# Optimization experiments

Hardware: AMD Instinct MI355X
Metric: run time of the kernel (lower is better)

The kernel has to match this reference:

```python
import jax, jax.numpy as jnp
import numpy as np

HIDDEN = 1024
HEADS = 16
HEAD_DIM = HIDDEN // HEADS
ROPE_BASE = 10000.0


def rope_cos_sin(seq_len, head_dim, dtype=jnp.float32):
    inv_freq = 1.0 / (ROPE_BASE ** (jnp.arange(0, head_dim, 2, dtype=jnp.float32) / head_dim))
    t = jnp.arange(seq_len, dtype=jnp.float32)
    freqs = jnp.einsum('i,j->ij', t, inv_freq)          # [L, head_dim/2]
    emb = jnp.concatenate([freqs, freqs], axis=-1)       # [L, head_dim]
    return emb.astype(dtype), jnp.cos(emb).astype(dtype), jnp.sin(emb).astype(dtype)


def rotate_half(x):
    half = x.shape[-1] // 2
    return jnp.concatenate([-x[..., half:], x[..., :half]], axis=-1)


def setup_inputs() -> dict:
    key = jax.random.key(0)
    kx, kq, kk, kv, ko = jax.random.split(key, 5)
    B, L = 4, 2048
    scale = 1.0 / np.sqrt(HIDDEN)
    x = jax.random.normal(kx, (B, L, HIDDEN), dtype=jnp.float32)
    Wq = jax.random.normal(kq, (HIDDEN, HIDDEN), dtype=jnp.float32) * scale
    Wk = jax.random.normal(kk, (HIDDEN, HIDDEN), dtype=jnp.float32) * scale
    Wv = jax.random.normal(kv, (HIDDEN, HIDDEN), dtype=jnp.float32) * scale
    Wo = jax.random.normal(ko, (HIDDEN, HIDDEN), dtype=jnp.float32) * scale
    return {"x": x, "Wq": Wq, "Wk": Wk, "Wv": Wv, "Wo": Wo}


def reference(x, Wq, Wk, Wv, Wo):
    B, L, D = x.shape
    H, Hd = HEADS, HEAD_DIM
    # projections (nn.Linear: y = x @ W.T; weights here stored already as [out,in])
    q = (x @ Wq.T).reshape(B, L, H, Hd).transpose(0, 2, 1, 3)  # [B,H,L,Hd]
    k = (x @ Wk.T).reshape(B, L, H, Hd).transpose(0, 2, 1, 3)
    v = (x @ Wv.T).reshape(B, L, H, Hd).transpose(0, 2, 1, 3)
    _, cos, sin = rope_cos_sin(L, Hd, x.dtype)                  # [L, Hd]
    cos = cos[None, None, :, :]
    sin = sin[None, None, :, :]
    q = q * cos + rotate_half(q) * sin
    k = k * cos + rotate_half(k) * sin
    scores = jnp.einsum('bhqd,bhkd->bhqk', q, k) / np.sqrt(Hd)  # [B,H,L,L]
    attn = jax.nn.softmax(scores, axis=-1)
    out = jnp.einsum('bhqk,bhkd->bhqd', attn, v)                # [B,H,L,Hd]
    out = out.transpose(0, 2, 1, 3).reshape(B, L, D)
    return out @ Wo.T
```

## Files before the change

### kernel.cpp

```cpp
#include <hip/hip_runtime.h>
#include <math.h>

#define BB 4
#define LL 2048
#define DD 1024
#define HH 16
#define HD 64
#define BL (BB*LL)

typedef __attribute__((ext_vector_type(8))) short bf16x8;
typedef __attribute__((ext_vector_type(4))) short bf16x4;
typedef __attribute__((ext_vector_type(4))) float f32x4;

__device__ inline short f2bf(float f) {
    union { float f; unsigned u; } v; v.f = f;
    unsigned r = v.u + 0x7fffu + ((v.u >> 16) & 1u);
    return (short)(r >> 16);
}

__device__ inline unsigned pk_bf16(float a, float b) {
    union { float f; unsigned u; } x, y; x.f = a; y.f = b;
#if __has_builtin(__builtin_amdgcn_perm)
    return __builtin_amdgcn_perm(y.u, x.u, 0x07060302u);
#else
    return (x.u >> 16) | (y.u & 0xffff0000u);
#endif
}

__device__ inline float exp2x(float x) {
#if __has_builtin(__builtin_amdgcn_exp2f)
    return __builtin_amdgcn_exp2f(x);
#else
    return exp2f(x);
#endif
}

__device__ inline void gload_lds16(const void* g, void* l) {
    __builtin_amdgcn_global_load_lds(
        (const __attribute__((address_space(1))) unsigned int*)g,
        (__attribute__((address_space(3))) unsigned int*)l, 16, 0, 0);
}

#define NB_CASTX ((BL*DD)/2048)
#define NB_CASTW (4*((DD*DD)/2048))
#define NB_ROPE  256

__global__ __launch_bounds__(256) void prep_kernel(
    const float* __restrict__ x,
    const float* __restrict__ w0, const float* __restrict__ w1,
    const float* __restrict__ w2, const float* __restrict__ w3,
    short* __restrict__ xb, short* __restrict__ wout,
    float2* __restrict__ tab)
{
    const int bid = blockIdx.x;
    if (bid < NB_CASTX) {
        int i = (bid * 256 + threadIdx.x) * 8;
        float4 a = *(const float4*)(x + i);
        float4 b = *(const float4*)(x + i + 4);
        bf16x8 o;
        o[0]=f2bf(a.x); o[1]=f2bf(a.y); o[2]=f2bf(a.z); o[3]=f2bf(a.w);
        o[4]=f2bf(b.x); o[5]=f2bf(b.y); o[6]=f2bf(b.z); o[7]=f2bf(b.w);
        *(bf16x8*)(xb + i) = o;
    } else if (bid < NB_CASTX + NB_CASTW) {
        const int nw_blocks = (DD*DD) / 2048;
        int b2  = bid - NB_CASTX;
        int sel = b2 / nw_blocks;
        int blk = b2 % nw_blocks;
        const float* in = (sel == 0) ? w0 : (sel == 1) ? w1 : (sel == 2) ? w2 : w3;
        int i = (blk * 256 + threadIdx.x) * 8;
        float4 a = *(const float4*)(in + i);
        float4 b = *(const float4*)(in + i + 4);
        bf16x8 o;
        o[0]=f2bf(a.x); o[1]=f2bf(a.y); o[2]=f2bf(a.z); o[3]=f2bf(a.w);
        o[4]=f2bf(b.x); o[5]=f2bf(b.y); o[6]=f2bf(b.z); o[7]=f2bf(b.w);
        *(bf16x8*)(wout + (size_t)sel * DD * DD + i) = o;
    } else {
        int idx = (bid - NB_CASTX - NB_CASTW) * 256 + threadIdx.x;
        int lq = idx >> 5, f = idx & 31;
        float inv = __expf((float)f * (-9.210340371976184f / 32.0f));
        float s, c;
        sincosf((float)lq * inv, &s, &c);
        tab[idx] = make_float2(c, s);
    }
}

__device__ inline void gemm_bt_128(const short* __restrict__ A,
                                   const short* __restrict__ B,
                                   short* Ash, short* Bsh,
                                   int i0, int n0, f32x4 (&acc)[4][4])
{
    const int t  = threadIdx.x;
    const int w  = t >> 6;
    const int l  = t & 63;
    const int g  = (t >> 4) & 3;
    const int ln = t & 15;
    const int rh = (w >> 1) * 64;
    const int ch = (w & 1) * 64;
    const int srow = w * 8 + (l >> 3);
    const int skol = ((l & 7) ^ (l >> 3)) * 8;
    const int rsw  = 8 * (ln & 7);

    for (int k0 = 0; k0 < DD; k0 += 64) {
        __syncthreads();
        const short* ga = A + (size_t)(i0 + srow) * DD + k0 + skol;
        const short* gb = B + (size_t)(n0 + srow) * DD + k0 + skol;
        short* la = Ash + w * 512;
        short* lb = Bsh + w * 512;
        #pragma unroll
        for (int j = 0; j < 4; ++j) {
            gload_lds16(ga + j * 32 * DD, la + j * 2048);
            gload_lds16(gb + j * 32 * DD, lb + j * 2048);
        }
        __syncthreads();

        #pragma unroll
        for (int kk = 0; kk < 2; ++kk) {
            bf16x8 af[4], bfr[4];
            #pragma unroll
            for (int mi = 0; mi < 4; ++mi)
                af[mi] = *(const bf16x8*)(Ash + (rh + mi*16 + ln)*64 + ((kk*32 + 8*g) ^ rsw));
            #pragma unroll
            for (int nj = 0; nj < 4; ++nj)
                bfr[nj] = *(const bf16x8*)(Bsh + (ch + nj*16 + ln)*64 + ((kk*32 + 8*g) ^ rsw));
            #pragma unroll
            for (int mi = 0; mi < 4; ++mi)
                #pragma unroll
                for (int nj = 0; nj < 4; ++nj)
                    acc[mi][nj] = __builtin_amdgcn_mfma_f32_16x16x32_bf16(
                        af[mi], bfr[nj], acc[mi][nj], 0, 0, 0);
        }
    }
}

__global__ __launch_bounds__(256, 4) void qkv_mfma_kernel(
    const short* __restrict__ xb, const short* __restrict__ Wqb,
    const short* __restrict__ Wkb, const short* __restrict__ Wvb,
    const float2* __restrict__ rope_tab,
    short* __restrict__ Qo, short* __restrict__ Ko, short* __restrict__ Vo)
{
    __shared__ short Ash[128*64];
    __shared__ short Bsh[128*64];

    const int gid = blockIdx.x;
    const int r8  = gid & 7;
    const int u   = gid >> 3;
    const int i_idx = r8 * 8 + (u & 7);
    const int nz  = u >> 3;
    const int n_idx = nz & 7;
    const int z   = nz >> 3;

    const short* Wm = (z == 0) ? Wqb : ((z == 1) ? Wkb : Wvb);
    const int i0 = i_idx * 128;
    const int n0 = n_idx * 128;

    f32x4 acc[4][4];
    #pragma unroll
    for (int mi = 0; mi < 4; ++mi)
        #pragma unroll
        for (int nj = 0; nj < 4; ++nj) acc[mi][nj] = (f32x4){0.f,0.f,0.f,0.f};

    gemm_bt_128(xb, Wm, Ash, Bsh, i0, n0, acc);

    const int t  = threadIdx.x;
    const int w  = t >> 6;
    const int g  = (t >> 4) & 3;
    const int ln = t & 15;
    const int rh = (w >> 1) * 64;

    if (z == 2) {
        short* buf = Ash;
        const int b = i0 >> 11, l0 = i0 & (LL - 1);
        const int d = t >> 2;
        const int c = t & 3;
        const int dk = d & 7;
        #pragma unroll
        for (int hp = 0; hp < 2; ++hp) {
            __syncthreads();
            if ((w & 1) == hp) {
                #pragma unroll
                for (int nj = 0; nj < 4; ++nj)
                    #pragma unroll
                    for (int mi = 0; mi < 4; ++mi)
                        #pragma unroll
                        for (int r = 0; r < 4; ++r)
                            buf[(nj*16 + ln)*136 + rh + mi*16 + 4*g + r]
                                = f2bf(acc[mi][nj][r]);
            }
            __syncthreads();
            short* dst = Vo + ((size_t)((b*HH + n_idx*2 + hp)*HD + d)) * LL + l0;
            #pragma unroll
            for (int j = 0; j < 4; ++j) {
                const short* src = buf + d*136 + c*8 + j*32;
                bf16x4 lo = *(const bf16x4*)(src);
                bf16x4 hi = *(const bf16x4*)(src + 4);
                const int tb = (j >> 1) * 64;
                const int hb = j & 1;
                const int aa = c >> 1;
                const int g0 = (c & 1) * 2;
                const int gi1 = 2*g0 + hb;
                *(bf16x4*)(dst + tb + ((gi1     ^ dk) << 3) + aa*4) = lo;
                *(bf16x4*)(dst + tb + (((gi1+2) ^ dk) << 3) + aa*4) = hi;
            }
        }
    } else {
        const int h = n_idx * 2 + (w & 1);
        short* Om = (z == 0) ? Qo : Ko;
        const float sc = (z == 0) ? 0.180336880111112f : 1.0f;
        const int gi0 = ln >> 3;
        const int wi  = ln & 7;
        #pragma unroll
        for (int mi = 0; mi < 4; ++mi)
            #pragma unroll
            for (int r = 0; r < 4; ++r) {
                int i = i0 + rh + mi*16 + 4*g + r;
                int b = i >> 11, lq = i & (LL - 1);
                float2 cs0 = rope_tab[lq*32 + ln];
                float2 cs1 = rope_tab[lq*32 + ln + 16];
                float r0 = (acc[mi][0][r]*cs0.x - acc[mi][2][r]*cs0.y) * sc;
                float r2 = (acc[mi][2][r]*cs0.x + acc[mi][0][r]*cs0.y) * sc;
                float r1 = (acc[mi][1][r]*cs1.x - acc[mi][3][r]*cs1.y) * sc;
                float r3 = (acc[mi][3][r]*cs1.x + acc[mi][1][r]*cs1.y) * sc;
                size_t base = ((size_t)(b*HH + h) * LL + lq) * HD;
                int xk = (z == 0) ? 0 : ((4*g + r) & 7);
                Om[base + (((gi0    ) ^ xk) << 3) + wi] = f2bf(r0);
                Om[base + (((gi0 + 2) ^ xk) << 3) + wi] = f2bf(r1);
                Om[base + (((gi0 + 4) ^ xk) << 3) + wi] = f2bf(r2);
                Om[base + (((gi0 + 6) ^ xk) << 3) + wi] = f2bf(r3);
            }
    }
}

__global__ __launch_bounds__(256) void attn_kernel(
    const short* __restrict__ Q, const short* __restrict__ K,
    const short* __restrict__ VT, short* __restrict__ AO)
{
    __shared__ short Ksh[64*64];
    __shared__ short VTs[64*64];

    const int t  = threadIdx.x;
    const int w  = t >> 6;
    const int l  = t & 63;
    const int g  = l >> 4;
    const int ln = l & 15;

    const int bh = blockIdx.x;
    const int q0 = blockIdx.y * 128;
    const short* Qb  = Q  + ((size_t)bh * LL + q0 + w*32) * HD;
    const short* Kb  = K  + (size_t)bh * LL * HD;
    const short* VTb = VT + (size_t)bh * HD * LL;

    bf16x8 qb[2][2];
    #pragma unroll
    for (int qi = 0; qi < 2; ++qi) {
        qb[qi][0] = *(const bf16x8*)(Qb + (size_t)(qi*16 + ln)*HD + 8*g);
        qb[qi][1] = *(const bf16x8*)(Qb + (size_t)(qi*16 + ln)*HD + 32 + 8*g);
    }

    const bf16x8 ONES = { (short)0x3F80, (short)0x3F80, (short)0x3F80, (short)0x3F80,
                          (short)0x3F80, (short)0x3F80, (short)0x3F80, (short)0x3F80 };

    f32x4 O[2][4];
    #pragma unroll
    for (int qi = 0; qi < 2; ++qi)
        #pragma unroll
        for (int db = 0; db < 4; ++db) O[qi][db] = (f32x4){0.f,0.f,0.f,0.f};
    f32x4 lsum[2];
    lsum[0] = (f32x4){0.f,0.f,0.f,0.f};
    lsum[1] = (f32x4){0.f,0.f,0.f,0.f};

    const int srow = l >> 3;
    const int scol = (l & 7) * 8;
    short* kdst = Ksh + w*1024;
    short* vdst = VTs + w*1024;
    const int lx = ln & 7;

    for (int kt = 0; kt < LL; kt += 64) {
        __syncthreads();
        const short* gk = Kb  + (size_t)(kt + w*16 + srow)*HD + scol;
        const short* gv = VTb + (size_t)(w*16 + srow)*LL + kt + scol;
        gload_lds16(gk,        kdst);
        gload_lds16(gk + 8*HD, kdst + 512);
        gload_lds16(gv,        vdst);
        gload_lds16(gv + 8*LL, vdst + 512);
        __syncthreads();

        unsigned pf[2][4][2];
        #pragma unroll
        for (int kb = 0; kb < 4; ++kb) {
            bf16x8 ka0 = *(const bf16x8*)(Ksh + (kb*16 + ln)*64 + ((g       ^ lx) << 3));
            bf16x8 ka1 = *(const bf16x8*)(Ksh + (kb*16 + ln)*64 + (((g + 4) ^ lx) << 3));
            #pragma unroll
            for (int qi = 0; qi < 2; ++qi) {
                f32x4 S = (f32x4){0.f,0.f,0.f,0.f};
                S = __builtin_amdgcn_mfma_f32_16x16x32_bf16(ka0, qb[qi][0], S, 0, 0, 0);
                S = __builtin_amdgcn_mfma_f32_16x16x32_bf16(ka1, qb[qi][1], S, 0, 0, 0);
                float p0 = exp2x(S[0]), p1 = exp2x(S[1]);
                float p2 = exp2x(S[2]), p3 = exp2x(S[3]);
                pf[qi][kb][0] = pk_bf16(p0, p1);
                pf[qi][kb][1] = pk_bf16(p2, p3);
            }
        }

        bf16x8 pa[2][2];
        #pragma unroll
        for (int qi = 0; qi < 2; ++qi)
            #pragma unroll
            for (int hb = 0; hb < 2; ++hb) {
                union { unsigned u[4]; bf16x8 v; } a;
                a.u[0] = pf[qi][2*hb][0];   a.u[1] = pf[qi][2*hb][1];
                a.u[2] = pf[qi][2*hb+1][0]; a.u[3] = pf[qi][2*hb+1][1];
                pa[qi][hb] = a.v;
            }

        #pragma unroll
        for (int hb = 0; hb < 2; ++hb) {
            lsum[0] = __builtin_amdgcn_mfma_f32_16x16x32_bf16(pa[0][hb], ONES, lsum[0], 0, 0, 0);
            lsum[1] = __builtin_amdgcn_mfma_f32_16x16x32_bf16(pa[1][hb], ONES, lsum[1], 0, 0, 0);
        }

        #pragma unroll
        for (int hb = 0; hb < 2; ++hb) {
            #pragma unroll
            for (int db = 0; db < 4; ++db) {
                bf16x8 vf = *(const bf16x8*)(VTs + (db*16 + ln)*64 + (((2*g + hb) ^ lx) << 3));
                O[0][db] = __builtin_amdgcn_mfma_f32_16x16x32_bf16(pa[0][hb], vf, O[0][db], 0, 0, 0);
                O[1][db] = __builtin_amdgcn_mfma_f32_16x16x32_bf16(pa[1][hb], vf, O[1][db], 0, 0, 0);
            }
        }
    }

    const int b = bh >> 4, h = bh & 15;
    #pragma unroll
    for (int qi = 0; qi < 2; ++qi) {
        #pragma unroll
        for (int r = 0; r < 4; ++r) {
            float inv = 1.0f / lsum[qi][r];
            int q = q0 + w*32 + qi*16 + 4*g + r;
            size_t base = ((size_t)(b*LL + q)) * DD + h*HD;
            #pragma unroll
            for (int db = 0; db < 4; ++db)
                AO[base + db*16 + ln] = f2bf(O[qi][db][r] * inv);
        }
    }
}

__global__ __launch_bounds__(256, 4) void oproj_mfma_kernel(
    const short* __restrict__ A, const short* __restrict__ Wob,
    float* __restrict__ out)
{
    __shared__ short Ash[128*64];
    __shared__ short Bsh[128*64];

    const int gid = blockIdx.x;
    const int r8  = gid & 7;
    const int u   = gid >> 3;
    const int i_idx = r8 * 8 + (u & 7);
    const int n_idx = u >> 3;
    const int i0 = i_idx * 128;
    const int n0 = n_idx * 128;

    f32x4 acc[4][4];
    #pragma unroll
    for (int mi = 0; mi < 4; ++mi)
        #pragma unroll
        for (int nj = 0; nj < 4; ++nj) acc[mi][nj] = (f32x4){0.f,0.f,0.f,0.f};

    gemm_bt_128(A, Wob, Ash, Bsh, i0, n0, acc);

    const int t  = threadIdx.x;
    const int w  = t >> 6;
    const int g  = (t >> 4) & 3;
    const int ln = t & 15;
    const int rh = (w >> 1) * 64;
    const int ch = (w & 1) * 64;

    #pragma unroll
    for (int mi = 0; mi < 4; ++mi)
        #pragma unroll
        for (int r = 0; r < 4; ++r) {
            size_t base = (size_t)(i0 + rh + mi*16 + 4*g + r) * DD + n0 + ch;
            #pragma unroll
            for (int nj = 0; nj < 4; ++nj)
                out[base + nj*16 + ln] = acc[mi][nj][r];
        }
}

extern "C" void kernel_launch(void* const* d_in, const int* in_sizes, int n_in,
                              void* d_out, int out_size, void* d_ws, size_t ws_size,
                              hipStream_t stream) {
    const float* x  = (const float*)d_in[0];
    const float* Wq = (const float*)d_in[1];
    const float* Wk = (const float*)d_in[2];
    const float* Wv = (const float*)d_in[3];
    const float* Wo = (const float*)d_in[4];
    float* out = (float*)d_out;

    const size_t n_x = (size_t)BL * DD;
    const size_t n_w = (size_t)DD * DD;
    short* xb  = (short*)d_ws;
    short* Wqb = xb  + n_x;
    short* Wkb = Wqb + n_w;
    short* Wvb = Wkb + n_w;
    short* Wob = Wvb + n_w;
    short* Q   = Wob + n_w;
    short* K   = Q   + n_x;
    short* VTg = K   + n_x;
    short* AOb = VTg + n_x;
    float2* tab = (float2*)(AOb + n_x);

    prep_kernel<<<NB_CASTX + NB_CASTW + NB_ROPE, 256, 0, stream>>>(
        x, Wq, Wk, Wv, Wo, xb, Wqb, tab);

    qkv_mfma_kernel<<<1536, 256, 0, stream>>>(xb, Wqb, Wkb, Wvb, tab, Q, K, VTg);

    dim3 g2(BB*HH, LL/128);
    attn_kernel<<<g2, 256, 0, stream>>>(Q, K, VTg, AOb);

    oproj_mfma_kernel<<<512, 256, 0, stream>>>(AOb, Wob, out);
}
```

Measured before the change: 251.9 us.

## Double-buffer GEMM K-loop in LDS with 32-wide stages to overlap loads

Reworks the shared bf16 GEMM main loop used by the QKV and output projections. It now keeps two 32-column K stages in LDS and issues the global-to-LDS loads for the next stage before computing on the current one, so load latency overlaps with MFMA work. LDS use stays the same because the two 128x64 tiles become four 128x32 tiles. The XOR swizzle is dropped in favour of a plain 32-short row stride, which may add LDS bank conflicts on the fragment reads. The number of barriers per 64-wide K step stays at two, but each barrier now covers half the work.

```diff
diff --git a/kernel.cpp b/kernel.cpp
--- a/kernel.cpp
+++ b/kernel.cpp
@@ -84,9 +84,40 @@
     }
 }
 
+__device__ inline void stage32(const short* __restrict__ A,
+                               const short* __restrict__ B,
+                               short* la, short* lb,
+                               int i0, int n0, int k0, int srow, int scol)
+{
+    const short* ga = A + (size_t)(i0 + srow) * DD + k0 + scol;
+    const short* gb = B + (size_t)(n0 + srow) * DD + k0 + scol;
+    gload_lds16(ga,           la);
+    gload_lds16(ga + 16 * DD, la + 512);
+    gload_lds16(gb,           lb);
+    gload_lds16(gb + 16 * DD, lb + 512);
+}
+
+__device__ inline void comp32(const short* Ab, const short* Bb,
+                              int rh, int ch, int g, int ln, f32x4 (&acc)[4][4])
+{
+    bf16x8 af[4], bfr[4];
+    #pragma unroll
+    for (int mi = 0; mi < 4; ++mi)
+        af[mi] = *(const bf16x8*)(Ab + (rh + mi*16 + ln)*32 + 8*g);
+    #pragma unroll
+    for (int nj = 0; nj < 4; ++nj)
+        bfr[nj] = *(const bf16x8*)(Bb + (ch + nj*16 + ln)*32 + 8*g);
+    #pragma unroll
+    for (int mi = 0; mi < 4; ++mi)
+        #pragma unroll
+        for (int nj = 0; nj < 4; ++nj)
+            acc[mi][nj] = __builtin_amdgcn_mfma_f32_16x16x32_bf16(
+                af[mi], bfr[nj], acc[mi][nj], 0, 0, 0);
+}
+
 __device__ inline void gemm_bt_128(const short* __restrict__ A,
                                    const short* __restrict__ B,
-                                   short* Ash, short* Bsh,
+                                   short* S,
                                    int i0, int n0, f32x4 (&acc)[4][4])
 {
     const int t  = threadIdx.x;
@@ -96,39 +127,23 @@
     const int ln = t & 15;
     const int rh = (w >> 1) * 64;
     const int ch = (w & 1) * 64;
-    const int srow = w * 8 + (l >> 3);
-    const int skol = ((l & 7) ^ (l >> 3)) * 8;
-    const int rsw  = 8 * (ln & 7);
-
+    const int srow = w * 32 + (l >> 2);
+    const int scol = (l & 3) * 8;
+
+    short* A0 = S;           short* A1 = S + 4096;
+    short* B0 = S + 8192;    short* B1 = S + 12288;
+    short* la0 = A0 + w*1024; short* la1 = A1 + w*1024;
+    short* lb0 = B0 + w*1024; short* lb1 = B1 + w*1024;
+
+    stage32(A, B, la0, lb0, i0, n0, 0, srow, scol);
     for (int k0 = 0; k0 < DD; k0 += 64) {
         __syncthreads();
-        const short* ga = A + (size_t)(i0 + srow) * DD + k0 + skol;
-        const short* gb = B + (size_t)(n0 + srow) * DD + k0 + skol;
-        short* la = Ash + w * 512;
-        short* lb = Bsh + w * 512;
-        #pragma unroll
-        for (int j = 0; j < 4; ++j) {
-            gload_lds16(ga + j * 32 * DD, la + j * 2048);
-            gload_lds16(gb + j * 32 * DD, lb + j * 2048);
-        }
+        stage32(A, B, la1, lb1, i0, n0, k0 + 32, srow, scol);
+        comp32(A0, B0, rh, ch, g, ln, acc);
         __syncthreads();
-
-        #pragma unroll
-        for (int kk = 0; kk < 2; ++kk) {
-            bf16x8 af[4], bfr[4];
-            #pragma unroll
-            for (int mi = 0; mi < 4; ++mi)
-                af[mi] = *(const bf16x8*)(Ash + (rh + mi*16 + ln)*64 + ((kk*32 + 8*g) ^ rsw));
-            #pragma unroll
-            for (int nj = 0; nj < 4; ++nj)
-                bfr[nj] = *(const bf16x8*)(Bsh + (ch + nj*16 + ln)*64 + ((kk*32 + 8*g) ^ rsw));
-            #pragma unroll
-            for (int mi = 0; mi < 4; ++mi)
-                #pragma unroll
-                for (int nj = 0; nj < 4; ++nj)
-                    acc[mi][nj] = __builtin_amdgcn_mfma_f32_16x16x32_bf16(
-                        af[mi], bfr[nj], acc[mi][nj], 0, 0, 0);
-        }
+        if (k0 + 64 < DD)
+            stage32(A, B, la0, lb0, i0, n0, k0 + 64, srow, scol);
+        comp32(A1, B1, rh, ch, g, ln, acc);
     }
 }
 
@@ -138,8 +153,7 @@
     const float2* __restrict__ rope_tab,
     short* __restrict__ Qo, short* __restrict__ Ko, short* __restrict__ Vo)
 {
-    __shared__ short Ash[128*64];
-    __shared__ short Bsh[128*64];
+    __shared__ short S[16384];
 
     const int gid = blockIdx.x;
     const int r8  = gid & 7;
@@ -159,7 +173,7 @@
         #pragma unroll
         for (int nj = 0; nj < 4; ++nj) acc[mi][nj] = (f32x4){0.f,0.f,0.f,0.f};
 
-    gemm_bt_128(xb, Wm, Ash, Bsh, i0, n0, acc);
+    gemm_bt_128(xb, Wm, S, i0, n0, acc);
 
     const int t  = threadIdx.x;
     const int w  = t >> 6;
@@ -168,7 +182,7 @@
     const int rh = (w >> 1) * 64;
 
     if (z == 2) {
-        short* buf = Ash;
+        short* buf = S;
         const int b = i0 >> 11, l0 = i0 & (LL - 1);
         const int d = t >> 2;
         const int c = t & 3;
@@ -348,8 +362,7 @@
     const short* __restrict__ A, const short* __restrict__ Wob,
     float* __restrict__ out)
 {
-    __shared__ short Ash[128*64];
-    __shared__ short Bsh[128*64];
+    __shared__ short S[16384];
 
     const int gid = blockIdx.x;
     const int r8  = gid & 7;
@@ -365,7 +378,7 @@
         #pragma unroll
         for (int nj = 0; nj < 4; ++nj) acc[mi][nj] = (f32x4){0.f,0.f,0.f,0.f};
 
-    gemm_bt_128(A, Wob, Ash, Bsh, i0, n0, acc);
+    gemm_bt_128(A, Wob, S, i0, n0, acc);
 
     const int t  = threadIdx.x;
     const int w  = t >> 6;
```

Result: no change. 255.4 us (+1.4%).

## Use 256x128 double-buffered GEMM tiles with 512 threads for projections

Applied to the files above, without the earlier changes.

Replaces the 128x128 single-buffered GEMM used by the QKV and output projections with a 256x128 tile computed by 8 waves. Next-k-step global-to-LDS loads go into a second buffer and are interleaved with MFMA phases, with setprio hints around the math. The aim is to hide load latency and reuse each B tile across more rows. In exchange, LDS per block grows to 96KB, occupancy drops, and the block count is halved, so the grid is less even across CUs.

```diff
diff --git a/kernel.cpp b/kernel.cpp
--- a/kernel.cpp
+++ b/kernel.cpp
@@ -84,73 +84,129 @@
     }
 }
 
-__device__ inline void gemm_bt_128(const short* __restrict__ A,
-                                   const short* __restrict__ B,
-                                   short* Ash, short* Bsh,
-                                   int i0, int n0, f32x4 (&acc)[4][4])
+__device__ inline void gemm256(const short* __restrict__ A,
+                               const short* __restrict__ B,
+                               short* S,
+                               int i0, int n0, f32x4 (&acc)[4][4])
 {
-    const int t  = threadIdx.x;
-    const int w  = t >> 6;
-    const int l  = t & 63;
-    const int g  = (t >> 4) & 3;
-    const int ln = t & 15;
-    const int rh = (w >> 1) * 64;
-    const int ch = (w & 1) * 64;
-    const int srow = w * 8 + (l >> 3);
-    const int skol = ((l & 7) ^ (l >> 3)) * 8;
-    const int rsw  = 8 * (ln & 7);
+    const int t   = threadIdx.x;
+    const int wid = t >> 6;
+    const int wr  = wid >> 1;
+    const int wc  = wid & 1;
+    const int l   = t & 63;
+    const int g   = (l >> 4) & 3;
+    const int ln  = l & 15;
+    const int rsw = 8 * (ln & 7);
+
+    short* A0 = S;
+    short* A1 = S + 16384;
+    short* B0 = S + 32768;
+    short* B1 = S + 40960;
+
+    const int srow = t >> 3;
+    const int sgr  = ((t & 7) ^ (srow & 7)) * 8;
+    const short* gA = A + (size_t)(i0 + srow) * DD + sgr;
+    const short* gB = B + (size_t)(n0 + srow) * DD + sgr;
+    const int lofs = wid * 512;
+
+    {
+        short* la = A0 + lofs; short* lb = B0 + lofs;
+        gload_lds16(gA,          la);
+        gload_lds16(gA +  64*DD, la + 4096);
+        gload_lds16(gA + 128*DD, la + 8192);
+        gload_lds16(gA + 192*DD, la + 12288);
+        gload_lds16(gB,          lb);
+        gload_lds16(gB +  64*DD, lb + 4096);
+    }
+    asm volatile("s_waitcnt vmcnt(0)" ::: "memory");
+    __builtin_amdgcn_s_barrier();
+
+    const int arow = wr*64 + ln;
+    const int brow = wc*64 + ln;
 
     for (int k0 = 0; k0 < DD; k0 += 64) {
-        __syncthreads();
-        const short* ga = A + (size_t)(i0 + srow) * DD + k0 + skol;
-        const short* gb = B + (size_t)(n0 + srow) * DD + k0 + skol;
-        short* la = Ash + w * 512;
-        short* lb = Bsh + w * 512;
-        #pragma unroll
-        for (int j = 0; j < 4; ++j) {
-            gload_lds16(ga + j * 32 * DD, la + j * 2048);
-            gload_lds16(gb + j * 32 * DD, lb + j * 2048);
-        }
-        __syncthreads();
-
-        #pragma unroll
-        for (int kk = 0; kk < 2; ++kk) {
-            bf16x8 af[4], bfr[4];
-            #pragma unroll
-            for (int mi = 0; mi < 4; ++mi)
-                af[mi] = *(const bf16x8*)(Ash + (rh + mi*16 + ln)*64 + ((kk*32 + 8*g) ^ rsw));
-            #pragma unroll
-            for (int nj = 0; nj < 4; ++nj)
-                bfr[nj] = *(const bf16x8*)(Bsh + (ch + nj*16 + ln)*64 + ((kk*32 + 8*g) ^ rsw));
-            #pragma unroll
-            for (int mi = 0; mi < 4; ++mi)
-                #pragma unroll
-                for (int nj = 0; nj < 4; ++nj)
-                    acc[mi][nj] = __builtin_amdgcn_mfma_f32_16x16x32_bf16(
-                        af[mi], bfr[nj], acc[mi][nj], 0, 0, 0);
-        }
-    }
-}
-
-__global__ __launch_bounds__(256, 4) void qkv_mfma_kernel(
+        short* Ab = (k0 & 64) ? A1 : A0;
+        short* Bb = (k0 & 64) ? B1 : B0;
+        short* An = (k0 & 64) ? A0 : A1;
+        short* Bn = (k0 & 64) ? B0 : B1;
+        const bool pf = (k0 + 64 < DD);
+
+        bf16x8 bfr[4][2], af0[2][2];
+        #pragma unroll
+        for (int nj = 0; nj < 4; ++nj)
+            #pragma unroll
+            for (int kk = 0; kk < 2; ++kk)
+                bfr[nj][kk] = *(const bf16x8*)(Bb + (brow + nj*16)*64 + ((kk*32 + 8*g) ^ rsw));
+        #pragma unroll
+        for (int mi = 0; mi < 2; ++mi)
+            #pragma unroll
+            for (int kk = 0; kk < 2; ++kk)
+                af0[mi][kk] = *(const bf16x8*)(Ab + (arow + mi*16)*64 + ((kk*32 + 8*g) ^ rsw));
+        if (pf) {
+            const short* ga = gA + k0 + 64;
+            short* la = An + lofs;
+            gload_lds16(ga,          la);
+            gload_lds16(ga +  64*DD, la + 4096);
+            gload_lds16(ga + 128*DD, la + 8192);
+            gload_lds16(ga + 192*DD, la + 12288);
+        }
+        __builtin_amdgcn_s_barrier();
+        __builtin_amdgcn_s_setprio(1);
+        #pragma unroll
+        for (int mi = 0; mi < 2; ++mi)
+            #pragma unroll
+            for (int nj = 0; nj < 4; ++nj) {
+                acc[mi][nj] = __builtin_amdgcn_mfma_f32_16x16x32_bf16(af0[mi][0], bfr[nj][0], acc[mi][nj], 0, 0, 0);
+                acc[mi][nj] = __builtin_amdgcn_mfma_f32_16x16x32_bf16(af0[mi][1], bfr[nj][1], acc[mi][nj], 0, 0, 0);
+            }
+        __builtin_amdgcn_s_setprio(0);
+        __builtin_amdgcn_s_barrier();
+
+        bf16x8 af1[2][2];
+        #pragma unroll
+        for (int mi = 0; mi < 2; ++mi)
+            #pragma unroll
+            for (int kk = 0; kk < 2; ++kk)
+                af1[mi][kk] = *(const bf16x8*)(Ab + (arow + (mi+2)*16)*64 + ((kk*32 + 8*g) ^ rsw));
+        if (pf) {
+            const short* gb = gB + k0 + 64;
+            short* lb = Bn + lofs;
+            gload_lds16(gb,         lb);
+            gload_lds16(gb + 64*DD, lb + 4096);
+        }
+        __builtin_amdgcn_s_barrier();
+        __builtin_amdgcn_s_setprio(1);
+        #pragma unroll
+        for (int mi = 0; mi < 2; ++mi)
+            #pragma unroll
+            for (int nj = 0; nj < 4; ++nj) {
+                acc[mi+2][nj] = __builtin_amdgcn_mfma_f32_16x16x32_bf16(af1[mi][0], bfr[nj][0], acc[mi+2][nj], 0, 0, 0);
+                acc[mi+2][nj] = __builtin_amdgcn_mfma_f32_16x16x32_bf16(af1[mi][1], bfr[nj][1], acc[mi+2][nj], 0, 0, 0);
+            }
+        __builtin_amdgcn_s_setprio(0);
+        if (pf) asm volatile("s_waitcnt vmcnt(0)" ::: "memory");
+        __builtin_amdgcn_s_barrier();
+    }
+}
+
+__global__ __launch_bounds__(512, 2) void qkv_mfma_kernel(
     const short* __restrict__ xb, const short* __restrict__ Wqb,
     const short* __restrict__ Wkb, const short* __restrict__ Wvb,
     const float2* __restrict__ rope_tab,
     short* __restrict__ Qo, short* __restrict__ Ko, short* __restrict__ Vo)
 {
-    __shared__ short Ash[128*64];
-    __shared__ short Bsh[128*64];
+    __shared__ short S[49152];
 
     const int gid = blockIdx.x;
     const int r8  = gid & 7;
     const int u   = gid >> 3;
-    const int i_idx = r8 * 8 + (u & 7);
-    const int nz  = u >> 3;
+    const int i_idx = r8 * 4 + (u & 3);
+    const int nz  = u >> 2;
     const int n_idx = nz & 7;
     const int z   = nz >> 3;
 
     const short* Wm = (z == 0) ? Wqb : ((z == 1) ? Wkb : Wvb);
-    const int i0 = i_idx * 128;
+    const int i0 = i_idx * 256;
     const int n0 = n_idx * 128;
 
     f32x4 acc[4][4];
@@ -159,43 +215,46 @@
         #pragma unroll
         for (int nj = 0; nj < 4; ++nj) acc[mi][nj] = (f32x4){0.f,0.f,0.f,0.f};
 
-    gemm_bt_128(xb, Wm, Ash, Bsh, i0, n0, acc);
-
-    const int t  = threadIdx.x;
-    const int w  = t >> 6;
-    const int g  = (t >> 4) & 3;
-    const int ln = t & 15;
-    const int rh = (w >> 1) * 64;
+    gemm256(xb, Wm, S, i0, n0, acc);
+
+    const int t   = threadIdx.x;
+    const int wid = t >> 6;
+    const int wr  = wid >> 1;
+    const int wc  = wid & 1;
+    const int l   = t & 63;
+    const int g   = (l >> 4) & 3;
+    const int ln  = l & 15;
 
     if (z == 2) {
-        short* buf = Ash;
+        short* buf = S;
         const int b = i0 >> 11, l0 = i0 & (LL - 1);
-        const int d = t >> 2;
-        const int c = t & 3;
+        const int d = t >> 3;
+        const int c = t & 7;
         const int dk = d & 7;
+        __syncthreads();
         #pragma unroll
         for (int hp = 0; hp < 2; ++hp) {
             __syncthreads();
-            if ((w & 1) == hp) {
+            if (wc == hp) {
                 #pragma unroll
                 for (int nj = 0; nj < 4; ++nj)
                     #pragma unroll
                     for (int mi = 0; mi < 4; ++mi)
                         #pragma unroll
                         for (int r = 0; r < 4; ++r)
-                            buf[(nj*16 + ln)*136 + rh + mi*16 + 4*g + r]
+                            buf[(nj*16 + ln)*264 + wr*64 + mi*16 + 4*g + r]
                                 = f2bf(acc[mi][nj][r]);
             }
             __syncthreads();
             short* dst = Vo + ((size_t)((b*HH + n_idx*2 + hp)*HD + d)) * LL + l0;
             #pragma unroll
             for (int j = 0; j < 4; ++j) {
-                const short* src = buf + d*136 + c*8 + j*32;
+                const short* src = buf + d*264 + c*8 + j*64;
                 bf16x4 lo = *(const bf16x4*)(src);
                 bf16x4 hi = *(const bf16x4*)(src + 4);
-                const int tb = (j >> 1) * 64;
-                const int hb = j & 1;
-                const int aa = c >> 1;
+                const int tb = j * 64;
+                const int hb = c >> 2;
+                const int aa = (c >> 1) & 1;
                 const int g0 = (c & 1) * 2;
                 const int gi1 = 2*g0 + hb;
                 *(bf16x4*)(dst + tb + ((gi1     ^ dk) << 3) + aa*4) = lo;
@@ -203,7 +262,7 @@
             }
         }
     } else {
-        const int h = n_idx * 2 + (w & 1);
+        const int h = n_idx * 2 + wc;
         short* Om = (z == 0) ? Qo : Ko;
         const float sc = (z == 0) ? 0.180336880111112f : 1.0f;
         const int gi0 = ln >> 3;
@@ -212,7 +271,7 @@
         for (int mi = 0; mi < 4; ++mi)
             #pragma unroll
             for (int r = 0; r < 4; ++r) {
-                int i = i0 + rh + mi*16 + 4*g + r;
+                int i = i0 + wr*64 + mi*16 + 4*g + r;
                 int b = i >> 11, lq = i & (LL - 1);
                 float2 cs0 = rope_tab[lq*32 + ln];
                 float2 cs1 = rope_tab[lq*32 + ln + 16];
@@ -291,11 +350,11 @@
             bf16x8 ka1 = *(const bf16x8*)(Ksh + (kb*16 + ln)*64 + (((g + 4) ^ lx) << 3));
             #pragma unroll
             for (int qi = 0; qi < 2; ++qi) {
-                f32x4 S = (f32x4){0.f,0.f,0.f,0.f};
-                S = __builtin_amdgcn_mfma_f32_16x16x32_bf16(ka0, qb[qi][0], S, 0, 0, 0);
-                S = __builtin_amdgcn_mfma_f32_16x16x32_bf16(ka1, qb[qi][1], S, 0, 0, 0);
-                float p0 = exp2x(S[0]), p1 = exp2x(S[1]);
-                float p2 = exp2x(S[2]), p3 = exp2x(S[3]);
+                f32x4 Sv = (f32x4){0.f,0.f,0.f,0.f};
+                Sv = __builtin_amdgcn_mfma_f32_16x16x32_bf16(ka0, qb[qi][0], Sv, 0, 0, 0);
+                Sv = __builtin_amdgcn_mfma_f32_16x16x32_bf16(ka1, qb[qi][1], Sv, 0, 0, 0);
+                float p0 = exp2x(Sv[0]), p1 = exp2x(Sv[1]);
+                float p2 = exp2x(Sv[2]), p3 = exp2x(Sv[3]);
                 pf[qi][kb][0] = pk_bf16(p0, p1);
                 pf[qi][kb][1] = pk_bf16(p2, p3);
             }
@@ -344,19 +403,18 @@
     }
 }
 
-__global__ __launch_bounds__(256, 4) void oproj_mfma_kernel(
+__global__ __launch_bounds__(512, 2) void oproj_mfma_kernel(
     const short* __restrict__ A, const short* __restrict__ Wob,
     float* __restrict__ out)
 {
-    __shared__ short Ash[128*64];
-    __shared__ short Bsh[128*64];
+    __shared__ short S[49152];
 
     const int gid = blockIdx.x;
     const int r8  = gid & 7;
     const int u   = gid >> 3;
-    const int i_idx = r8 * 8 + (u & 7);
-    const int n_idx = u >> 3;
-    const int i0 = i_idx * 128;
+    const int i_idx = r8 * 4 + (u & 3);
+    const int n_idx = u >> 2;
+    const int i0 = i_idx * 256;
     const int n0 = n_idx * 128;
 
     f32x4 acc[4][4];
@@ -365,20 +423,21 @@
         #pragma unroll
         for (int nj = 0; nj < 4; ++nj) acc[mi][nj] = (f32x4){0.f,0.f,0.f,0.f};
 
-    gemm_bt_128(A, Wob, Ash, Bsh, i0, n0, acc);
-
-    const int t  = threadIdx.x;
-    const int w  = t >> 6;
-    const int g  = (t >> 4) & 3;
-    const int ln = t & 15;
-    const int rh = (w >> 1) * 64;
-    const int ch = (w & 1) * 64;
+    gemm256(A, Wob, S, i0, n0, acc);
+
+    const int t   = threadIdx.x;
+    const int wid = t >> 6;
+    const int wr  = wid >> 1;
+    const int wc  = wid & 1;
+    const int l   = t & 63;
+    const int g   = (l >> 4) & 3;
+    const int ln  = l & 15;
 
     #pragma unroll
     for (int mi = 0; mi < 4; ++mi)
         #pragma unroll
         for (int r = 0; r < 4; ++r) {
-            size_t base = (size_t)(i0 + rh + mi*16 + 4*g + r) * DD + n0 + ch;
+            size_t base = (size_t)(i0 + wr*64 + mi*16 + 4*g + r) * DD + n0 + wc*64;
             #pragma unroll
             for (int nj = 0; nj < 4; ++nj)
                 out[base + nj*16 + ln] = acc[mi][nj][r];
@@ -411,10 +470,10 @@
     prep_kernel<<<NB_CASTX + NB_CASTW + NB_ROPE, 256, 0, stream>>>(
         x, Wq, Wk, Wv, Wo, xb, Wqb, tab);
 
-    qkv_mfma_kernel<<<1536, 256, 0, stream>>>(xb, Wqb, Wkb, Wvb, tab, Q, K, VTg);
+    qkv_mfma_kernel<<<768, 512, 0, stream>>>(xb, Wqb, Wkb, Wvb, tab, Q, K, VTg);
 
     dim3 g2(BB*HH, LL/128);
     attn_kernel<<<g2, 256, 0, stream>>>(Q, K, VTg, AOb);
 
-    oproj_mfma_kernel<<<512, 256, 0, stream>>>(AOb, Wob, out);
-}
+    oproj_mfma_kernel<<<256, 512, 0, stream>>>(AOb, Wob, out);
+}
```

After: 258.8 us. 1.03x slower.
